# Optimization experiments

Measured on AMD Instinct MI355X. Metric: run time of the kernel, lower is better.

Reference implementation:

```python
import jax, jax.numpy as jnp
import numpy as np

B = 8192
D = 1024
NUM_HEADS = 16
HEAD_DIM = D // NUM_HEADS  # 64; only used as the softmax scale


def setup_inputs() -> dict:
    key = jax.random.key(0)
    ks = jax.random.split(key, 7)
    s = 1.0 / np.sqrt(D)
    return {
        "x": jax.random.normal(ks[0], (B, D), dtype=jnp.float32),
        "Wq": jax.random.normal(ks[1], (D, D), dtype=jnp.float32) * s,
        "bq": jax.random.normal(ks[2], (D,), dtype=jnp.float32) * s,
        "Wk": jax.random.normal(ks[3], (D, D), dtype=jnp.float32) * s,
        "bk": jax.random.normal(ks[4], (D,), dtype=jnp.float32) * s,
        "Wv": jax.random.normal(ks[5], (D, D), dtype=jnp.float32) * s,
        "bv": jax.random.normal(ks[6], (D,), dtype=jnp.float32) * s,
    }


def reference(x, Wq, bq, Wk, bk, Wv, bv):
    # Faithful to the torch module: x is 2D [B, D]; attention is over the batch axis.
    # nn.Linear computes x @ W.T + b
    Q = x @ Wq.T + bq            # [B, D]
    K = x @ Wk.T + bk            # [B, D]
    V = x @ Wv.T + bv            # [B, D]
    scale = 1.0 / jnp.sqrt(jnp.float32(HEAD_DIM))
    energy = (Q @ K.T) * scale   # [B, B]
    attn = jax.nn.softmax(energy, axis=-1)
    out = attn @ V               # [B, D]
    # torch: x.permute(0,1).contiguous().view(B, seq_len, -1) -> [B, D, 1]
    return out.reshape(B, D, 1)
```

## Files before the change

kernel.cpp:

```cpp
#include <hip/hip_runtime.h>
#include <hip/hip_bf16.h>

typedef _Float16 half_t;
typedef _Float16 f16x8 __attribute__((ext_vector_type(8)));
typedef _Float16 f16x4 __attribute__((ext_vector_type(4)));
typedef float f32x4 __attribute__((ext_vector_type(4)));
typedef float f32x16 __attribute__((ext_vector_type(16)));

#define B_ROWS 8192
#define D_DIM  1024

__device__ __forceinline__ void gload_lds16(const void* g, void* l)
{
    __builtin_amdgcn_global_load_lds((const __attribute__((address_space(1))) void*)g,
                                     (__attribute__((address_space(3))) void*)l, 16, 0, 0);
}

__global__ __launch_bounds__(256)
void cvt_f32_f16(const float* __restrict__ in, half_t* __restrict__ out, int n)
{
    int i = (blockIdx.x * 256 + threadIdx.x) * 4;
    int stride = gridDim.x * 256 * 4;
    for (; i < n; i += stride) {
        float4 v = *(const float4*)&in[i];
        f16x4 o;
        o[0] = (half_t)v.x; o[1] = (half_t)v.y; o[2] = (half_t)v.z; o[3] = (half_t)v.w;
        *(f16x4*)&out[i] = o;
    }
}

__global__ __launch_bounds__(256)
void transpose_h(const half_t* __restrict__ in, half_t* __restrict__ out, int R, int C)
{
    __shared__ half_t t[64][65];
    int tilesC = C >> 6;
    int bc = blockIdx.x % tilesC;
    int br = blockIdx.x / tilesC;
    int r0 = br * 64, c0 = bc * 64;
    for (int e = threadIdx.x; e < 64 * 64; e += 256) {
        int r = e >> 6, c = e & 63;
        t[r][c] = in[(size_t)(r0 + r) * C + (c0 + c)];
    }
    __syncthreads();
    for (int e = threadIdx.x; e < 64 * 64; e += 256) {
        int r = e >> 6, c = e & 63;
        out[(size_t)(c0 + r) * R + (r0 + c)] = t[c][r];
    }
}

template<int EPI>
__device__ __forceinline__ void gemm8_core(
    const half_t* __restrict__ A, const half_t* __restrict__ Bm,
    const float* __restrict__ bias, void* __restrict__ Out,
    int lda, int ldb, int ldc, float scale,
    int row0, int col0, int ktile0, int nkt)
{
    __shared__ __align__(16) half_t As[4 * 8192];
    __shared__ __align__(16) half_t Bs[4 * 8192];

    const int tid  = threadIdx.x;
    const int lane = tid & 63;
    const int wid  = tid >> 6;
    const int wr   = wid >> 2;
    const int wcn  = wid & 3;
    const int l31  = lane & 31;
    const int l32  = lane >> 5;

    const int trow  = tid >> 3;
    const int tslot = (tid & 7) ^ (trow & 7);
    const char* Apan[2] = { (const char*)(A + (size_t)row0 * lda),
                            (const char*)(A + (size_t)(row0 + 128) * lda) };
    const char* Bpan[2] = { (const char*)(Bm + (size_t)col0 * ldb),
                            (const char*)(Bm + (size_t)(col0 + 128) * ldb) };
    const size_t aoff[2] = { (size_t)trow * lda * 2 + (size_t)tslot * 16,
                             (size_t)(trow + 64) * lda * 2 + (size_t)tslot * 16 };
    const size_t boff[2] = { (size_t)trow * ldb * 2 + (size_t)tslot * 16,
                             (size_t)(trow + 64) * ldb * 2 + (size_t)tslot * 16 };
    const int dstb[2] = { tid * 16, 8192 + tid * 16 };

    auto stageA = [&](int h, int s, int buf) {
        char* d = (char*)(As + (buf * 2 + h) * 8192);
        const char* g = Apan[h] + (size_t)(ktile0 + s) * 128;
        gload_lds16(g + aoff[0], d + dstb[0]);
        gload_lds16(g + aoff[1], d + dstb[1]);
    };
    auto stageB = [&](int h, int s, int buf) {
        char* d = (char*)(Bs + (buf * 2 + h) * 8192);
        const char* g = Bpan[h] + (size_t)(ktile0 + s) * 128;
        gload_lds16(g + boff[0], d + dstb[0]);
        gload_lds16(g + boff[1], d + dstb[1]);
    };
    auto rdA = [&](int mm, int kc, const half_t* base) -> f16x8 {
        int rih  = wr * 64 + mm * 32 + l31;
        int byte = rih * 128 + (((kc * 2 + l32) ^ (rih & 7)) << 4);
        return *(const f16x8*)((const char*)base + byte);
    };
    auto rdB = [&](int kc, const half_t* base) -> f16x8 {
        int rih  = wcn * 32 + l31;
        int byte = rih * 128 + (((kc * 2 + l32) ^ (rih & 7)) << 4);
        return *(const f16x8*)((const char*)base + byte);
    };

    f32x16 acc[2][2][2] = {};
    f16x8 af[2][4];
    f16x8 bfP[4], bfQ[4];

    {
        int s1 = (nkt > 1) ? 1 : 0;
        stageA(0, 0, 0); stageB(0, 0, 0); stageA(1, 0, 0); stageB(1, 0, 0);
        stageA(0, s1, 1); stageB(0, s1, 1);
    }
    asm volatile("s_waitcnt vmcnt(4)" ::: "memory");
    asm volatile("s_barrier" ::: "memory");

    for (int t = 0; t < nkt; ++t) {
        const int buf = t & 1;
        const half_t* A0 = As + (buf * 2 + 0) * 8192;
        const half_t* A1 = As + (buf * 2 + 1) * 8192;
        const half_t* B0 = Bs + (buf * 2 + 0) * 8192;
        const half_t* B1 = Bs + (buf * 2 + 1) * 8192;
        int t1  = t + 1; int t1s = (t1 < nkt) ? t1 : nkt - 1; int b1 = t1 & 1;
        int t2  = t + 2; int t2s = (t2 < nkt) ? t2 : nkt - 1;

        #pragma unroll
        for (int mm = 0; mm < 2; ++mm)
            #pragma unroll
            for (int kc = 0; kc < 4; ++kc) af[mm][kc] = rdA(mm, kc, A0);
        #pragma unroll
        for (int kc = 0; kc < 4; ++kc) bfP[kc] = rdB(kc, B0);
        stageA(1, t1s, b1);
        asm volatile("s_barrier" ::: "memory");
        __builtin_amdgcn_s_setprio(1);
        #pragma unroll
        for (int kc = 0; kc < 4; ++kc)
            #pragma unroll
            for (int mm = 0; mm < 2; ++mm)
                acc[0][mm][0] = __builtin_amdgcn_mfma_f32_32x32x16_f16(af[mm][kc], bfP[kc], acc[0][mm][0], 0, 0, 0);
        __builtin_amdgcn_s_setprio(0);
        asm volatile("s_barrier" ::: "memory");

        #pragma unroll
        for (int kc = 0; kc < 4; ++kc) bfQ[kc] = rdB(kc, B1);
        stageB(1, t1s, b1);
        asm volatile("s_barrier" ::: "memory");
        __builtin_amdgcn_s_setprio(1);
        #pragma unroll
        for (int kc = 0; kc < 4; ++kc)
            #pragma unroll
            for (int mm = 0; mm < 2; ++mm)
                acc[0][mm][1] = __builtin_amdgcn_mfma_f32_32x32x16_f16(af[mm][kc], bfQ[kc], acc[0][mm][1], 0, 0, 0);
        __builtin_amdgcn_s_setprio(0);
        asm volatile("s_barrier" ::: "memory");

        #pragma unroll
        for (int mm = 0; mm < 2; ++mm)
            #pragma unroll
            for (int kc = 0; kc < 4; ++kc) af[mm][kc] = rdA(mm, kc, A1);
        stageA(0, t2s, buf);
        asm volatile("s_barrier" ::: "memory");
        __builtin_amdgcn_s_setprio(1);
        #pragma unroll
        for (int kc = 0; kc < 4; ++kc)
            #pragma unroll
            for (int mm = 0; mm < 2; ++mm)
                acc[1][mm][0] = __builtin_amdgcn_mfma_f32_32x32x16_f16(af[mm][kc], bfP[kc], acc[1][mm][0], 0, 0, 0);
        __builtin_amdgcn_s_setprio(0);
        asm volatile("s_barrier" ::: "memory");

        stageB(0, t2s, buf);
        asm volatile("s_barrier" ::: "memory");
        __builtin_amdgcn_s_setprio(1);
        #pragma unroll
        for (int kc = 0; kc < 4; ++kc)
            #pragma unroll
            for (int mm = 0; mm < 2; ++mm)
                acc[1][mm][1] = __builtin_amdgcn_mfma_f32_32x32x16_f16(af[mm][kc], bfQ[kc], acc[1][mm][1], 0, 0, 0);
        __builtin_amdgcn_s_setprio(0);
        asm volatile("s_waitcnt vmcnt(4)" ::: "memory");
        asm volatile("s_barrier" ::: "memory");
    }

    #pragma unroll
    for (int h = 0; h < 2; ++h) {
        #pragma unroll
        for (int mm = 0; mm < 2; ++mm) {
            int r0 = row0 + h * 128 + wr * 64 + mm * 32 + 4 * l32;
            #pragma unroll
            for (int nh = 0; nh < 2; ++nh) {
                int gcol = col0 + nh * 128 + wcn * 32 + l31;
                float badd = (EPI == 0) ? bias[gcol] : 0.0f;
                #pragma unroll
                for (int g = 0; g < 16; ++g) {
                    int row = r0 + (g & 3) + 8 * (g >> 2);
                    float v = acc[h][mm][nh][g] * scale + badd;
                    size_t idx = (size_t)row * ldc + gcol;
                    if (EPI == 2) ((float*)Out)[idx] = v;
                    else          ((half_t*)Out)[idx] = (half_t)v;
                }
            }
        }
    }
}

template<int EPI, int REMAP>
__global__ __launch_bounds__(512, 2)
void gemm8(const half_t* __restrict__ A, const half_t* __restrict__ Bm,
           const float* __restrict__ bias, void* __restrict__ Out,
           int lda, int ldb, int ldc, float scale, int nkt)
{
    int bx, by;
    if (REMAP) {
        int L = blockIdx.y * gridDim.x + blockIdx.x;
        int s = L >> 8;
        int u = L & 255;
        int xcd  = u & 7;
        int slot = u >> 3;
        by = (s >> 1) * 16 + xcd * 2 + (slot >> 4);
        bx = (s & 1) * 16 + (slot & 15);
    } else {
        int nwg = gridDim.x * gridDim.y;
        int bid = blockIdx.y * gridDim.x + blockIdx.x;
        if ((nwg & 7) == 0) { int c = nwg >> 3; bid = (bid & 7) * c + (bid >> 3); }
        bx = bid % gridDim.x; by = bid / gridDim.x;
    }
    gemm8_core<EPI>(A, Bm, bias, Out, lda, ldb, ldc, scale, by * 256, bx * 256, 0, nkt);
}

__global__ __launch_bounds__(512, 2)
void gemm8_qkv(const half_t* __restrict__ xh,
               const half_t* __restrict__ Wq, const half_t* __restrict__ Wk, const half_t* __restrict__ Wv,
               const float* __restrict__ bq, const float* __restrict__ bk, const float* __restrict__ bv,
               half_t* __restrict__ Q, half_t* __restrict__ K, half_t* __restrict__ V)
{
    int z = blockIdx.z;
    const half_t* W = (z == 0) ? Wq : (z == 1) ? Wk : Wv;
    const float*  b = (z == 0) ? bq : (z == 1) ? bk : bv;
    half_t*       O = (z == 0) ? Q  : (z == 1) ? K  : V;
    gemm8_core<0>(xh, W, b, O, D_DIM, D_DIM, D_DIM, 1.0f,
                  blockIdx.y * 256, blockIdx.x * 256, 0, D_DIM / 64);
}

__global__ __launch_bounds__(512, 2)
void gemm8_pv(const half_t* __restrict__ S, const half_t* __restrict__ Vt,
              float* __restrict__ part0, float* __restrict__ part1)
{
    int h = blockIdx.z * 128 + blockIdx.y * 4 + blockIdx.x;
    int l = (h & 7) * 32 + (h >> 3);
    int z  = l >> 7;
    int r  = l & 127;
    int by = r >> 2;
    int bx = r & 3;
    float* O = z ? part1 : part0;
    gemm8_core<2>(S, Vt, nullptr, O, B_ROWS, B_ROWS, D_DIM, 1.0f,
                  by * 256, bx * 256, z * (B_ROWS / 128), B_ROWS / 128);
}

__global__ __launch_bounds__(256)
void add_f32(const float* __restrict__ a, float* __restrict__ out, int n)
{
    int i = (blockIdx.x * 256 + threadIdx.x) * 4;
    int stride = gridDim.x * 256 * 4;
    for (; i < n; i += stride) {
        float4 x = *(const float4*)&out[i];
        float4 y = *(const float4*)&a[i];
        x.x += y.x; x.y += y.y; x.z += y.z; x.w += y.w;
        *(float4*)&out[i] = x;
    }
}

__global__ __launch_bounds__(256)
void softmax_rows(half_t* __restrict__ S, int ncol)
{
    const int row = blockIdx.x;
    half_t* srow = S + (size_t)row * ncol;
    const int tid = threadIdx.x;

    float ev[32];
    float m = -1e30f;
    #pragma unroll
    for (int it = 0; it < 4; ++it) {
        int j = it * 2048 + tid * 8;
        f16x8 v = *(const f16x8*)&srow[j];
        #pragma unroll
        for (int t = 0; t < 8; ++t) {
            float f = (float)v[t];
            ev[it * 8 + t] = f;
            m = fmaxf(m, f);
        }
    }
    #pragma unroll
    for (int o = 32; o; o >>= 1) m = fmaxf(m, __shfl_down(m, o));
    __shared__ float redm[8];
    __shared__ float reds[8];
    if ((tid & 63) == 0) redm[tid >> 6] = m;
    __syncthreads();
    m = fmaxf(fmaxf(redm[0], redm[1]), fmaxf(redm[2], redm[3]));

    float s = 0.0f;
    #pragma unroll
    for (int e = 0; e < 32; ++e) {
        float ex = __expf(ev[e] - m);
        ev[e] = ex;
        s += ex;
    }
    #pragma unroll
    for (int o = 32; o; o >>= 1) s += __shfl_down(s, o);
    if ((tid & 63) == 0) reds[tid >> 6] = s;
    __syncthreads();
    s = reds[0] + reds[1] + reds[2] + reds[3];
    float inv = 1.0f / s;

    #pragma unroll
    for (int it = 0; it < 4; ++it) {
        int j = it * 2048 + tid * 8;
        f16x8 o8;
        #pragma unroll
        for (int t = 0; t < 8; ++t) o8[t] = (half_t)(ev[it * 8 + t] * inv);
        *(f16x8*)&srow[j] = o8;
    }
}

extern "C" void kernel_launch(void* const* d_in, const int* in_sizes, int n_in,
                              void* d_out, int out_size, void* d_ws, size_t ws_size,
                              hipStream_t stream)
{
    const float* x  = (const float*)d_in[0];
    const float* Wq = (const float*)d_in[1];
    const float* bq = (const float*)d_in[2];
    const float* Wk = (const float*)d_in[3];
    const float* bk = (const float*)d_in[4];
    const float* Wv = (const float*)d_in[5];
    const float* bv = (const float*)d_in[6];
    float* out = (float*)d_out;

    const int Bb = B_ROWS, Dd = D_DIM;

    char* w = (char*)d_ws;
    size_t off = 0;
    auto carve = [&](size_t bytes) {
        void* p = w + off;
        off += (bytes + 255) & ~(size_t)255;
        return p;
    };
    half_t* xh  = (half_t*)carve((size_t)Bb * Dd * 2);
    half_t* Wqh = (half_t*)carve((size_t)Dd * Dd * 2);
    half_t* Wkh = (half_t*)carve((size_t)Dd * Dd * 2);
    half_t* Wvh = (half_t*)carve((size_t)Dd * Dd * 2);
    half_t* Qh  = (half_t*)carve((size_t)Bb * Dd * 2);
    half_t* Kh  = (half_t*)carve((size_t)Bb * Dd * 2);
    half_t* Vh  = (half_t*)carve((size_t)Bb * Dd * 2);
    half_t* S   = (half_t*)carve((size_t)Bb * Bb * 2);
    half_t* Vt  = xh;
    float*  part1 = (float*)Qh;

    cvt_f32_f16<<<2048, 256, 0, stream>>>(x,  xh,  Bb * Dd);
    cvt_f32_f16<<<1024, 256, 0, stream>>>(Wq, Wqh, Dd * Dd);
    cvt_f32_f16<<<1024, 256, 0, stream>>>(Wk, Wkh, Dd * Dd);
    cvt_f32_f16<<<1024, 256, 0, stream>>>(Wv, Wvh, Dd * Dd);

    dim3 gqkv(Dd / 256, Bb / 256, 3);
    gemm8_qkv<<<gqkv, 512, 0, stream>>>(xh, Wqh, Wkh, Wvh, bq, bk, bv, Qh, Kh, Vh);

    transpose_h<<<(Dd / 64) * (Bb / 64), 256, 0, stream>>>(Vh, Vt, Bb, Dd);

    dim3 gs(Bb / 256, Bb / 256);
    gemm8<1, 1><<<gs, 512, 0, stream>>>(Qh, Kh, nullptr, S, Dd, Dd, Bb, 0.125f, Dd / 64);

    softmax_rows<<<Bb, 256, 0, stream>>>(S, Bb);

    dim3 gpv(Dd / 256, Bb / 256, 2);
    gemm8_pv<<<gpv, 512, 0, stream>>>(S, Vt, out, part1);
    add_f32<<<2048, 256, 0, stream>>>(part1, out, Bb * Dd);
}
```

Baseline: 438.4 us.

## Restructure GEMM main loop pipeline to cut barriers and prefetch B fragments early

Reorders the double-buffered GEMM main loop. The B0 fragment for the next tile is now read at the end of the current iteration, and the next tile's quarter-tiles are staged one at a time during each MFMA phase. Roughly half of the s_barrier calls are dropped, replaced by finer vmcnt waits. This aims to reduce synchronization stalls and overlap loads with MFMA work, at the risk of LDS read/write hazards if the wait counts are off.

```diff
diff --git a/kernel.cpp b/kernel.cpp
--- a/kernel.cpp
+++ b/kernel.cpp
@@ -105,31 +105,33 @@
     f16x8 af[2][4];
     f16x8 bfP[4], bfQ[4];
 
+    stageB(0, 0, 0); stageA(0, 0, 0); stageB(1, 0, 0); stageA(1, 0, 0);
+    asm volatile("s_waitcnt vmcnt(6)" ::: "memory");
+    asm volatile("s_barrier" ::: "memory");
     {
-        int s1 = (nkt > 1) ? 1 : 0;
-        stageA(0, 0, 0); stageB(0, 0, 0); stageA(1, 0, 0); stageB(1, 0, 0);
-        stageA(0, s1, 1); stageB(0, s1, 1);
-    }
-    asm volatile("s_waitcnt vmcnt(4)" ::: "memory");
-    asm volatile("s_barrier" ::: "memory");
+        const half_t* B0 = Bs;
+        #pragma unroll
+        for (int kc = 0; kc < 4; ++kc) bfP[kc] = rdB(kc, B0);
+    }
 
     for (int t = 0; t < nkt; ++t) {
-        const int buf = t & 1;
-        const half_t* A0 = As + (buf * 2 + 0) * 8192;
-        const half_t* A1 = As + (buf * 2 + 1) * 8192;
-        const half_t* B0 = Bs + (buf * 2 + 0) * 8192;
-        const half_t* B1 = Bs + (buf * 2 + 1) * 8192;
-        int t1  = t + 1; int t1s = (t1 < nkt) ? t1 : nkt - 1; int b1 = t1 & 1;
-        int t2  = t + 2; int t2s = (t2 < nkt) ? t2 : nkt - 1;
-
-        #pragma unroll
-        for (int mm = 0; mm < 2; ++mm)
-            #pragma unroll
-            for (int kc = 0; kc < 4; ++kc) af[mm][kc] = rdA(mm, kc, A0);
-        #pragma unroll
-        for (int kc = 0; kc < 4; ++kc) bfP[kc] = rdB(kc, B0);
-        stageA(1, t1s, b1);
+        const int buf  = t & 1;
+        const int bufn = buf ^ 1;
+        const half_t* A0  = As + (buf * 2 + 0) * 8192;
+        const half_t* A1  = As + (buf * 2 + 1) * 8192;
+        const half_t* B1c = Bs + (buf * 2 + 1) * 8192;
+        const half_t* B0n = Bs + (bufn * 2 + 0) * 8192;
+        const int t1s = (t + 1 < nkt) ? t + 1 : nkt - 1;
+
+        asm volatile("s_waitcnt vmcnt(2)" ::: "memory");
         asm volatile("s_barrier" ::: "memory");
+        #pragma unroll
+        for (int kc = 0; kc < 4; ++kc)
+            #pragma unroll
+            for (int mm = 0; mm < 2; ++mm) af[mm][kc] = rdA(mm, kc, A0);
+        #pragma unroll
+        for (int kc = 0; kc < 4; ++kc) bfQ[kc] = rdB(kc, B1c);
+        stageB(0, t1s, bufn);
         __builtin_amdgcn_s_setprio(1);
         #pragma unroll
         for (int kc = 0; kc < 4; ++kc)
@@ -137,12 +139,8 @@
             for (int mm = 0; mm < 2; ++mm)
                 acc[0][mm][0] = __builtin_amdgcn_mfma_f32_32x32x16_f16(af[mm][kc], bfP[kc], acc[0][mm][0], 0, 0, 0);
         __builtin_amdgcn_s_setprio(0);
-        asm volatile("s_barrier" ::: "memory");
-
-        #pragma unroll
-        for (int kc = 0; kc < 4; ++kc) bfQ[kc] = rdB(kc, B1);
-        stageB(1, t1s, b1);
-        asm volatile("s_barrier" ::: "memory");
+
+        stageA(0, t1s, bufn);
         __builtin_amdgcn_s_setprio(1);
         #pragma unroll
         for (int kc = 0; kc < 4; ++kc)
@@ -150,14 +148,14 @@
             for (int mm = 0; mm < 2; ++mm)
                 acc[0][mm][1] = __builtin_amdgcn_mfma_f32_32x32x16_f16(af[mm][kc], bfQ[kc], acc[0][mm][1], 0, 0, 0);
         __builtin_amdgcn_s_setprio(0);
+
+        asm volatile("s_waitcnt vmcnt(4)" ::: "memory");
         asm volatile("s_barrier" ::: "memory");
-
-        #pragma unroll
-        for (int mm = 0; mm < 2; ++mm)
-            #pragma unroll
-            for (int kc = 0; kc < 4; ++kc) af[mm][kc] = rdA(mm, kc, A1);
-        stageA(0, t2s, buf);
-        asm volatile("s_barrier" ::: "memory");
+        #pragma unroll
+        for (int kc = 0; kc < 4; ++kc)
+            #pragma unroll
+            for (int mm = 0; mm < 2; ++mm) af[mm][kc] = rdA(mm, kc, A1);
+        stageB(1, t1s, bufn);
         __builtin_amdgcn_s_setprio(1);
         #pragma unroll
         for (int kc = 0; kc < 4; ++kc)
@@ -165,10 +163,12 @@
             for (int mm = 0; mm < 2; ++mm)
                 acc[1][mm][0] = __builtin_amdgcn_mfma_f32_32x32x16_f16(af[mm][kc], bfP[kc], acc[1][mm][0], 0, 0, 0);
         __builtin_amdgcn_s_setprio(0);
+
+        asm volatile("s_waitcnt vmcnt(4)" ::: "memory");
         asm volatile("s_barrier" ::: "memory");
-
-        stageB(0, t2s, buf);
-        asm volatile("s_barrier" ::: "memory");
+        #pragma unroll
+        for (int kc = 0; kc < 4; ++kc) bfP[kc] = rdB(kc, B0n);
+        stageA(1, t1s, bufn);
         __builtin_amdgcn_s_setprio(1);
         #pragma unroll
         for (int kc = 0; kc < 4; ++kc)
@@ -176,8 +176,6 @@
             for (int mm = 0; mm < 2; ++mm)
                 acc[1][mm][1] = __builtin_amdgcn_mfma_f32_32x32x16_f16(af[mm][kc], bfQ[kc], acc[1][mm][1], 0, 0, 0);
         __builtin_amdgcn_s_setprio(0);
-        asm volatile("s_waitcnt vmcnt(4)" ::: "memory");
-        asm volatile("s_barrier" ::: "memory");
     }
 
     #pragma unroll
```

After: 458.9 us. +4.7%, slower.
